# Kernel optimization log

Measured on AMD Instinct MI355X. Metric: run time of the kernel, lower is better.

Reference implementation:

```python
import jax, jax.numpy as jnp
import numpy as np

B, C, N = 2, 6, 2048      # batch, channels (xyz+3 extra), points per cloud
K, NS = 64, 32            # top-k keypoints, ball-query group size
D = 32                    # deep feature dim (num_feat)
RADIUS = 1.0              # ball query radius (sample_and_group)
VR, VS = 1.0, 0.4         # voxelize range / step -> 6^3 = 216 candidates


def setup_inputs() -> dict:
    key = jax.random.key(0)
    ks = jax.random.split(key, 16)
    rn = lambda k, s, sc=1.0: jax.random.normal(k, s, dtype=jnp.float32) * sc
    Q, _ = jnp.linalg.qr(jax.random.normal(ks[2], (3, 3), dtype=jnp.float32))
    return {
        "src_pts": rn(ks[0], (B, C, N)),
        "tgt_pts": rn(ks[1], (B, C, N)),
        "R_init": Q,
        "t_init": rn(ks[3], (1, 3), 0.1),
        "W1": rn(ks[4], (C, 64), 0.2), "b1": jnp.zeros((64,), jnp.float32),
        "W2": rn(ks[5], (64, D), 0.2), "b2": jnp.zeros((D,), jnp.float32),
        "Wwl": rn(ks[6], (D, 1), 0.2), "bwl": jnp.zeros((1,), jnp.float32),
        "W3": rn(ks[7], (3 + D, 64), 0.2), "b3": jnp.zeros((64,), jnp.float32),
        "W4": rn(ks[8], (64, D), 0.2), "b4": jnp.zeros((D,), jnp.float32),
    }


def _fe(pts, W1, b1, W2, b2):
    # feat_extraction_layer: shared point-wise MLP. pts [B,C,N] -> xyz [B,N,3], feat [B,N,D]
    x = jnp.transpose(pts, (0, 2, 1))
    xyz = x[..., :3]
    f = jax.nn.relu(x @ W1 + b1)
    f = jax.nn.relu(f @ W2 + b2)
    return xyz, f


def _index_points(pts, idx):
    # pts [B,N,D], idx [B,K,S] -> [B,K,S,D]
    b = pts.shape[0]
    return pts[jnp.arange(b)[:, None, None], idx]


def _sqdist(a, b):
    # a [B,M,3], b [B,N,3] -> [B,M,N]
    return (jnp.sum(a * a, -1)[:, :, None] + jnp.sum(b * b, -1)[:, None, :]
            - 2.0 * jnp.einsum('bmd,bnd->bmn', a, b))


def reference(src_pts, tgt_pts, R_init, t_init, W1, b1, W2, b2, Wwl, bwl, W3, b3, W4, b4):
    b = src_pts.shape[0]
    # FE1 on source
    src_xyz, src_feat = _fe(src_pts, W1, b1, W2, b2)
    # weighting_layer: per-point saliency -> top-K keypoint indices
    w = (src_feat @ Wwl + bwl)[..., 0]                    # [B,N]
    _, kidx = jax.lax.top_k(w, K)                          # [B,K]
    src_T = jnp.transpose(src_pts, (0, 2, 1))              # [B,N,C]
    src_keypts = jnp.take_along_axis(src_T, kidx[:, :, None], axis=1)  # [B,K,C]
    centers = src_keypts[..., :3]
    # sample_and_group: ball query NS nearest-within-radius around each keypoint
    d2 = _sqdist(centers, src_xyz)                         # [B,K,N]
    negd, nn = jax.lax.top_k(-d2, NS)
    group_idx = jnp.where(-negd <= RADIUS ** 2, nn, nn[:, :, :1])
    grouped_xyz = _index_points(src_xyz, group_idx)        # [B,K,NS,3]
    keyfeats = _index_points(src_feat, group_idx)          # [B,K,NS,D]
    src_cat = jnp.concatenate([grouped_xyz - centers[:, :, None, :], keyfeats], -1)
    # FE1 on target
    tgt_xyz, tgt_feat = _fe(tgt_pts, W1, b1, W2, b2)
    # transform keypoints with initial pose, voxelize into candidate grid
    xform = jnp.einsum('ij,bkj->bki', R_init, centers) + t_init
    g = jnp.arange(int(2 * VR / VS) + 1, dtype=jnp.float32) * VS - VR   # 6 steps
    gx, gy, gz = jnp.meshgrid(g, g, g, indexing='ij')
    offs = jnp.stack([gx.ravel(), gy.ravel(), gz.ravel()], -1)          # [216,3]
    cand = xform[:, :, None, :] + offs                      # [B,K,216,3]
    nc = offs.shape[0]
    cand_flat = cand.reshape(b, K * nc, 3)
    # nearest target point per candidate -> gathered deep feature + relative offset
    d2t = _sqdist(cand_flat, tgt_xyz)                       # [B,K*216,N] (dominant buffer)
    nnt = jnp.argmin(d2t, axis=-1)                          # [B,K*216]
    nn_xyz = jnp.take_along_axis(tgt_xyz, nnt[:, :, None], axis=1)
    nn_feat = jnp.take_along_axis(tgt_feat, nnt[:, :, None], axis=1)
    rel = (nn_xyz - cand_flat).reshape(b, K, nc, 3)
    tgt_cat = jnp.concatenate([rel, nn_feat.reshape(b, K, nc, D)], -1)
    # DFE: shared MLP; src branch max-pools over the NS group
    dfe = lambda x: jax.nn.relu(jax.nn.relu(x @ W3 + b3) @ W4 + b4)
    src_dfe = jnp.max(dfe(src_cat), axis=2)                 # [B,K,D]
    tgt_dfe = dfe(tgt_cat)                                  # [B,K,216,D]
    # cpg: similarity -> softmax over candidates -> weighted centroid
    sim = jnp.einsum('bkd,bkcd->bkc', src_dfe, tgt_dfe)
    attn = jax.nn.softmax(sim, axis=-1)
    vcp = jnp.einsum('bkc,bkcd->bkd', attn, cand)           # [B,K,3]
    return src_keypts, vcp
```

## Files before the change

### kernel.cpp

```cpp
#include <hip/hip_runtime.h>
#include <math.h>

#define BB_ 2
#define CC_ 6
#define NN_ 2048
#define KK_ 64
#define NS_ 32
#define DD_ 32
#define NC_ 216
#define HH_ 64

#define OFF_SRC_PACK 0
#define OFF_TGT_PACK 16384
#define OFF_SRC_FEAT 32768
#define OFF_TGT_FEAT 163840
#define OFF_W        294912
#define OFF_CENTERS  299008
#define OFF_XFORM    299392
#define OFF_SRCDFE   299776
#define OFF_NNT      303872

__device__ __forceinline__ unsigned sortable_f32(float f) {
    unsigned u = __float_as_uint(f);
    return (u & 0x80000000u) ? ~u : (u | 0x80000000u);
}
__device__ __forceinline__ float unsortable_f32(unsigned s) {
    unsigned u = (s & 0x80000000u) ? (s ^ 0x80000000u) : ~s;
    return __uint_as_float(u);
}

__device__ __forceinline__ unsigned long long wave_sort64_asc(unsigned long long key, int lane) {
#pragma unroll
    for (int k = 2; k <= 64; k <<= 1) {
#pragma unroll
        for (int j = k >> 1; j > 0; j >>= 1) {
            unsigned long long other = __shfl_xor(key, j);
            bool lower = (lane & j) == 0;
            bool asc = (lane & k) == 0;
            bool takemin = (lower == asc);
            unsigned long long mn = key < other ? key : other;
            unsigned long long mx = key < other ? other : key;
            key = takemin ? mn : mx;
        }
    }
    return key;
}

__device__ __forceinline__ unsigned long long merge_keep_min64(unsigned long long a, unsigned long long b, int lane) {
    unsigned long long br = __shfl(b, 63 - lane);
    unsigned long long m = a < br ? a : br;
#pragma unroll
    for (int j = 32; j > 0; j >>= 1) {
        unsigned long long other = __shfl_xor(m, j);
        bool lower = (lane & j) == 0;
        unsigned long long mn = m < other ? m : other;
        unsigned long long mx = m < other ? other : m;
        m = lower ? mn : mx;
    }
    return m;
}

__device__ __forceinline__ void block_select64_16w(unsigned long long kA, unsigned long long kB,
                                                   unsigned long long* runs, int tid) {
    int w = tid >> 6, lane = tid & 63;
    kA = wave_sort64_asc(kA, lane);
    kB = wave_sort64_asc(kB, lane);
    unsigned long long m = merge_keep_min64(kA, kB, lane);
    runs[w * 64 + lane] = m;
    __syncthreads();
#pragma unroll
    for (int lvl = 8; lvl >= 1; lvl >>= 1) {
        unsigned long long r = 0;
        if (w < lvl) {
            unsigned long long a = runs[w * 64 + lane];
            unsigned long long b = runs[(w + lvl) * 64 + lane];
            r = merge_keep_min64(a, b, lane);
        }
        __syncthreads();
        if (w < lvl) runs[w * 64 + lane] = r;
        __syncthreads();
    }
}

__global__ void fe_kernel(const float* __restrict__ src, const float* __restrict__ tgt,
                          const float* __restrict__ W1, const float* __restrict__ b1,
                          const float* __restrict__ W2, const float* __restrict__ b2,
                          const float* __restrict__ Wwl, const float* __restrict__ bwl,
                          float* __restrict__ ws) {
    int tid = blockIdx.x * blockDim.x + threadIdx.x;
    if (tid >= 2 * BB_ * NN_) return;
    int cloud = tid / (BB_ * NN_);
    int r = tid - cloud * BB_ * NN_;
    int b = r / NN_, n = r % NN_;
    const float* pts = cloud ? tgt : src;
    float x[CC_];
#pragma unroll
    for (int c = 0; c < CC_; ++c) x[c] = pts[(b * CC_ + c) * NN_ + n];
    float bb;
    {
#pragma clang fp contract(off)
        bb = (x[0] * x[0] + x[1] * x[1]) + x[2] * x[2];
    }
    float4* pack = (float4*)(ws + (cloud ? OFF_TGT_PACK : OFF_SRC_PACK));
    pack[b * NN_ + n] = make_float4(x[0], x[1], x[2], bb);

    float h[HH_];
#pragma unroll
    for (int t = 0; t < HH_; ++t) {
        float s = b1[t];
#pragma unroll
        for (int c = 0; c < CC_; ++c) s += x[c] * W1[c * HH_ + t];
        h[t] = fmaxf(s, 0.f);
    }
    float* feat = ws + (cloud ? OFF_TGT_FEAT : OFF_SRC_FEAT) + (size_t)(b * NN_ + n) * DD_;
    float wsum = 0.f;
#pragma unroll 4
    for (int d = 0; d < DD_; ++d) {
        float s = b2[d];
#pragma unroll
        for (int t = 0; t < HH_; ++t) s += h[t] * W2[t * DD_ + d];
        s = fmaxf(s, 0.f);
        feat[d] = s;
        wsum += s * Wwl[d];
    }
    if (cloud == 0) (ws + OFF_W)[b * NN_ + n] = wsum + bwl[0];
}

__global__ void topk_kernel(const float* __restrict__ src, const float* __restrict__ R,
                            const float* __restrict__ t, float* __restrict__ ws,
                            float* __restrict__ out) {
    __shared__ unsigned long long runs[16 * 64];
    int b = blockIdx.x;
    int tid = threadIdx.x, w = tid >> 6, lane = tid & 63;
    const float* wv = ws + OFF_W + b * NN_;
    int jA = w * 128 + lane, jB = jA + 64;
    unsigned long long kA = ((unsigned long long)(~sortable_f32(wv[jA])) << 32) | (unsigned)jA;
    unsigned long long kB = ((unsigned long long)(~sortable_f32(wv[jB])) << 32) | (unsigned)jB;
    block_select64_16w(kA, kB, runs, tid);
    if (tid < KK_) {
        int bi = (int)(runs[tid] & 0xFFFFFFFFu);
        float c3[3];
#pragma unroll
        for (int c = 0; c < CC_; ++c) {
            float v = src[(b * CC_ + c) * NN_ + bi];
            out[(b * KK_ + tid) * CC_ + c] = v;
            if (c < 3) c3[c] = v;
        }
        float* cen = ws + OFF_CENTERS + (b * KK_ + tid) * 3;
        cen[0] = c3[0]; cen[1] = c3[1]; cen[2] = c3[2];
        float* xf = ws + OFF_XFORM + (b * KK_ + tid) * 3;
#pragma unroll
        for (int i = 0; i < 3; ++i) {
#pragma clang fp contract(off)
            xf[i] = ((R[i * 3 + 0] * c3[0] + R[i * 3 + 1] * c3[1]) + R[i * 3 + 2] * c3[2]) + t[i];
        }
    }
}

__global__ __launch_bounds__(576) void mid_kernel(const float* __restrict__ W3, const float* __restrict__ b3,
                                                  const float* __restrict__ W4, const float* __restrict__ b4,
                                                  float* __restrict__ ws) {
    __shared__ union U {
        float4 pk[NN_];
        struct {
            unsigned long long runs[8 * 64];
            float hs[NS_][HH_];
            float outs[NS_][DD_];
        } s;
    } u;
    int blk = blockIdx.x;
    int tid = threadIdx.x;
    if (blk < 2 * BB_ * KK_) {
        int bk = blk >> 1;
        int half = blk & 1;
        int b = bk / KK_;
        const float4* pack = (const float4*)(ws + OFF_TGT_PACK) + b * NN_;
        for (int j = tid; j < NN_; j += 576) {
            u.pk[j ^ ((j >> 6) & 7)] = pack[j];
        }
        const float* xf = ws + OFF_XFORM + bk * 3;
        float x0 = xf[0], x1 = xf[1], x2 = xf[2];
        __syncthreads();

        int lg = tid >> 5;
        int chunk = tid & 31;
        int grp = half * 18 + lg;
        int ix = grp / 6, iy = grp % 6;
        float cx = x0 + (ix * 0.4f - 1.0f);
        float cy = x1 + (iy * 0.4f - 1.0f);
        float cxy2;
        {
#pragma clang fp contract(off)
            cxy2 = cx * cx + cy * cy;
        }
        float m2x = -2.0f * cx, m2y = -2.0f * cy;
        float aaz[6], m2z[6];
#pragma unroll
        for (int z = 0; z < 6; ++z) {
            float cz = x2 + (z * 0.4f - 1.0f);
            {
#pragma clang fp contract(off)
                aaz[z] = cxy2 + cz * cz;
            }
            m2z[z] = -2.0f * cz;
        }
        float bv[6];
        int bi[6];
#pragma unroll
        for (int z = 0; z < 6; ++z) { bv[z] = INFINITY; bi[z] = 0; }
        int base = chunk * 64;
        int sw = chunk & 7;
        for (int i = 0; i < 64; ++i) {
            int j = base + i;
            float4 p = u.pk[base + (i ^ sw)];
            float txy;
            {
#pragma clang fp contract(off)
                txy = m2x * p.x + m2y * p.y;
            }
#pragma unroll
            for (int z = 0; z < 6; ++z) {
                float d2;
                {
#pragma clang fp contract(off)
                    d2 = (aaz[z] + p.w) + (txy + m2z[z] * p.z);
                }
                if (d2 < bv[z]) { bv[z] = d2; bi[z] = j; }
            }
        }
        int* nnt = (int*)ws + OFF_NNT + bk * NC_ + grp * 6;
#pragma unroll
        for (int z = 0; z < 6; ++z) {
            unsigned long long key = ((unsigned long long)sortable_f32(bv[z]) << 32) | (unsigned)bi[z];
#pragma unroll
            for (int m = 1; m <= 16; m <<= 1) {
                unsigned long long other = __shfl_xor(key, m);
                key = other < key ? other : key;
            }
            if (chunk == 0) nnt[z] = (int)(key & 0xFFFFFFFFu);
        }
    } else {
        int bk = blk - 2 * BB_ * KK_;
        int b = bk / KK_;
        int w = tid >> 6, lane = tid & 63;
        const float* cen = ws + OFF_CENTERS + bk * 3;
        float c0 = cen[0], c1 = cen[1], c2 = cen[2];
        float aa;
        {
#pragma clang fp contract(off)
            aa = (c0 * c0 + c1 * c1) + c2 * c2;
        }
        float m2x = -2.0f * c0, m2y = -2.0f * c1, m2z = -2.0f * c2;
        const float4* pack = (const float4*)(ws + OFF_SRC_PACK) + b * NN_;
        if (w < 8) {
            unsigned long long k4[4];
#pragma unroll
            for (int q = 0; q < 4; ++q) {
                int j = w * 256 + q * 64 + lane;
                float4 p = pack[j];
                float d2;
                {
#pragma clang fp contract(off)
                    d2 = (aa + p.w) + ((m2x * p.x + m2y * p.y) + m2z * p.z);
                }
                k4[q] = ((unsigned long long)sortable_f32(d2) << 32) | (unsigned)j;
            }
            unsigned long long m1 = merge_keep_min64(wave_sort64_asc(k4[0], lane),
                                                     wave_sort64_asc(k4[1], lane), lane);
            unsigned long long m2 = merge_keep_min64(wave_sort64_asc(k4[2], lane),
                                                     wave_sort64_asc(k4[3], lane), lane);
            u.s.runs[w * 64 + lane] = merge_keep_min64(m1, m2, lane);
        }
        __syncthreads();
#pragma unroll
        for (int lvl = 4; lvl >= 1; lvl >>= 1) {
            unsigned long long r = 0;
            if (w < lvl) {
                r = merge_keep_min64(u.s.runs[w * 64 + lane], u.s.runs[(w + lvl) * 64 + lane], lane);
            }
            __syncthreads();
            if (w < lvl) u.s.runs[w * 64 + lane] = r;
            __syncthreads();
        }
        const float* feats = ws + OFF_SRC_FEAT + (size_t)b * NN_ * DD_;
        unsigned long long key0 = u.s.runs[0];
        if (w < 8) {
#pragma unroll
            for (int ss = 0; ss < 4; ++ss) {
                int s = w * 4 + ss;
                unsigned long long key = u.s.runs[s];
                float dd = unsortable_f32((unsigned)(key >> 32));
                int j = (dd <= 1.0f) ? (int)(key & 0xFFFFFFFFu) : (int)(key0 & 0xFFFFFFFFu);
                float4 p = pack[j];
                float r0 = p.x - c0, r1 = p.y - c1, r2 = p.z - c2;
                const float* f = feats + (size_t)j * DD_;
                float acc = b3[lane] + r0 * W3[0 * HH_ + lane] + r1 * W3[1 * HH_ + lane] + r2 * W3[2 * HH_ + lane];
#pragma unroll 8
                for (int d = 0; d < DD_; ++d) acc += f[d] * W3[(3 + d) * HH_ + lane];
                u.s.hs[s][lane] = fmaxf(acc, 0.f);
            }
        }
        __syncthreads();
        for (int idx = tid; idx < NS_ * DD_; idx += 576) {
            int s2 = idx >> 5, di = idx & 31;
            float o = b4[di];
#pragma unroll 8
            for (int t2 = 0; t2 < HH_; ++t2) o += u.s.hs[s2][t2] * W4[t2 * DD_ + di];
            u.s.outs[s2][di] = fmaxf(o, 0.f);
        }
        __syncthreads();
        if (tid < DD_) {
            float m = -INFINITY;
#pragma unroll 8
            for (int s = 0; s < NS_; ++s) m = fmaxf(m, u.s.outs[s][tid]);
            (ws + OFF_SRCDFE)[bk * DD_ + tid] = m;
        }
    }
}

__global__ void simvcp_kernel(const float* __restrict__ W3, const float* __restrict__ b3,
                              const float* __restrict__ W4, const float* __restrict__ b4,
                              float* __restrict__ ws, float* __restrict__ out) {
    __shared__ float sims[NC_];
    int bk = blockIdx.x;
    int b = bk / KK_;
    int tid = threadIdx.x;
    const float* xf = ws + OFF_XFORM + bk * 3;
    if (tid < NC_) {
        int c = tid;
        int ix = c / 36, iy = (c / 6) % 6, iz = c % 6;
        float cx = xf[0] + (ix * 0.4f - 1.0f);
        float cy = xf[1] + (iy * 0.4f - 1.0f);
        float cz = xf[2] + (iz * 0.4f - 1.0f);
        int bi = ((const int*)ws)[OFF_NNT + bk * NC_ + c];
        float4 p = ((const float4*)(ws + OFF_TGT_PACK))[b * NN_ + bi];
        float x[3 + DD_];
        x[0] = p.x - cx; x[1] = p.y - cy; x[2] = p.z - cz;
        const float* f = ws + OFF_TGT_FEAT + ((size_t)b * NN_ + bi) * DD_;
#pragma unroll
        for (int d = 0; d < DD_; ++d) x[3 + d] = f[d];
        float o[DD_];
#pragma unroll
        for (int d = 0; d < DD_; ++d) o[d] = b4[d];
        for (int t = 0; t < HH_; ++t) {
            float acc = b3[t];
#pragma unroll
            for (int cc = 0; cc < 3 + DD_; ++cc) acc += x[cc] * W3[cc * HH_ + t];
            float ht = fmaxf(acc, 0.f);
#pragma unroll
            for (int d = 0; d < DD_; ++d) o[d] += ht * W4[t * DD_ + d];
        }
        const float* sd = ws + OFF_SRCDFE + bk * DD_;
        float sim = 0.f;
#pragma unroll
        for (int d = 0; d < DD_; ++d) sim += fmaxf(o[d], 0.f) * sd[d];
        sims[c] = sim;
    }
    __syncthreads();
    if (tid < 64) {
        int lane = tid;
        float m = -INFINITY;
        for (int c = lane; c < NC_; c += 64) m = fmaxf(m, sims[c]);
#pragma unroll
        for (int sh = 32; sh; sh >>= 1) m = fmaxf(m, __shfl_xor(m, sh));
        float se = 0.f, v0 = 0.f, v1 = 0.f, v2 = 0.f;
        for (int c = lane; c < NC_; c += 64) {
            float e = expf(sims[c] - m);
            int ix = c / 36, iy = (c / 6) % 6, iz = c % 6;
            se += e;
            v0 += e * (xf[0] + (ix * 0.4f - 1.0f));
            v1 += e * (xf[1] + (iy * 0.4f - 1.0f));
            v2 += e * (xf[2] + (iz * 0.4f - 1.0f));
        }
#pragma unroll
        for (int sh = 32; sh; sh >>= 1) {
            se += __shfl_xor(se, sh);
            v0 += __shfl_xor(v0, sh);
            v1 += __shfl_xor(v1, sh);
            v2 += __shfl_xor(v2, sh);
        }
        if (lane == 0) {
            float inv = 1.0f / se;
            float* oo = out + BB_ * KK_ * CC_ + bk * 3;
            oo[0] = v0 * inv;
            oo[1] = v1 * inv;
            oo[2] = v2 * inv;
        }
    }
}

extern "C" void kernel_launch(void* const* d_in, const int* in_sizes, int n_in,
                              void* d_out, int out_size, void* d_ws, size_t ws_size,
                              hipStream_t stream) {
    const float* src = (const float*)d_in[0];
    const float* tgt = (const float*)d_in[1];
    const float* R   = (const float*)d_in[2];
    const float* t   = (const float*)d_in[3];
    const float* W1  = (const float*)d_in[4];
    const float* b1  = (const float*)d_in[5];
    const float* W2  = (const float*)d_in[6];
    const float* b2  = (const float*)d_in[7];
    const float* Wwl = (const float*)d_in[8];
    const float* bwl = (const float*)d_in[9];
    const float* W3  = (const float*)d_in[10];
    const float* b3  = (const float*)d_in[11];
    const float* W4  = (const float*)d_in[12];
    const float* b4  = (const float*)d_in[13];
    float* ws  = (float*)d_ws;
    float* out = (float*)d_out;

    fe_kernel<<<(2 * BB_ * NN_ + 127) / 128, 128, 0, stream>>>(src, tgt, W1, b1, W2, b2, Wwl, bwl, ws);
    topk_kernel<<<BB_, 1024, 0, stream>>>(src, R, t, ws, out);
    mid_kernel<<<2 * BB_ * KK_ + BB_ * KK_, 576, 0, stream>>>(W3, b3, W4, b4, ws);
    simvcp_kernel<<<BB_ * KK_, 256, 0, stream>>>(W3, b3, W4, b4, ws, out);
}
```

Baseline: 82.53 us.

## Fuse four stage kernels into one cooperative kernel with grid syncs

Merges feature extraction, top-k selection, target nearest-neighbour search, source grouping/DFE and the similarity/softmax stage into a single cooperatively launched kernel of 256 blocks of 576 threads, separated by grid.sync barriers. The aim is to remove the launch gaps between the four separate kernels. The source-grouping work, which previously ran in its own blocks concurrently with the NN search, now runs after the NN search in half of the same blocks, so that part is serialized. Top-k now uses 8 waves of 4 keys each instead of 16 waves. The old four-kernel path is kept as a fallback if the cooperative launch fails. The merged kernel also risks higher register pressure under the 576-thread launch bound, plus the cost of each grid-wide barrier.

```diff
diff --git a/kernel.cpp b/kernel.cpp
--- a/kernel.cpp
+++ b/kernel.cpp
@@ -1,5 +1,8 @@
 #include <hip/hip_runtime.h>
+#include <hip/hip_cooperative_groups.h>
 #include <math.h>
+
+namespace cg = cooperative_groups;
 
 #define BB_ 2
 #define CC_ 6
@@ -60,25 +63,335 @@
     return m;
 }
 
-__device__ __forceinline__ void block_select64_16w(unsigned long long kA, unsigned long long kB,
-                                                   unsigned long long* runs, int tid) {
-    int w = tid >> 6, lane = tid & 63;
-    kA = wave_sort64_asc(kA, lane);
-    kB = wave_sort64_asc(kB, lane);
-    unsigned long long m = merge_keep_min64(kA, kB, lane);
-    runs[w * 64 + lane] = m;
+
+struct MegaLds {
+    union {
+        float4 pk[NN_];
+        struct {
+            unsigned long long runs[8 * 64];
+            float hs[NS_][HH_];
+            float outs[NS_][DD_];
+        } s;
+        float sims[NC_];
+    };
+};
+
+__global__ __launch_bounds__(576) void mega_kernel(
+        const float* __restrict__ src, const float* __restrict__ tgt,
+        const float* __restrict__ R, const float* __restrict__ t,
+        const float* __restrict__ W1, const float* __restrict__ b1,
+        const float* __restrict__ W2, const float* __restrict__ b2,
+        const float* __restrict__ Wwl, const float* __restrict__ bwl,
+        const float* __restrict__ W3, const float* __restrict__ b3,
+        const float* __restrict__ W4, const float* __restrict__ b4,
+        float* __restrict__ ws, float* __restrict__ out) {
+    cg::grid_group grid = cg::this_grid();
+    __shared__ MegaLds u;
+    int blk = blockIdx.x;
+    int tid = threadIdx.x;
+
+    {
+        int g = blk * 576 + tid;
+        if (g < 2 * BB_ * NN_) {
+            int cloud = g / (BB_ * NN_);
+            int r = g - cloud * BB_ * NN_;
+            int b = r / NN_, n = r % NN_;
+            const float* pts = cloud ? tgt : src;
+            float x[CC_];
+#pragma unroll
+            for (int c = 0; c < CC_; ++c) x[c] = pts[(b * CC_ + c) * NN_ + n];
+            float bb;
+            {
+#pragma clang fp contract(off)
+                bb = (x[0] * x[0] + x[1] * x[1]) + x[2] * x[2];
+            }
+            float4* pack = (float4*)(ws + (cloud ? OFF_TGT_PACK : OFF_SRC_PACK));
+            pack[b * NN_ + n] = make_float4(x[0], x[1], x[2], bb);
+            float h[HH_];
+#pragma unroll
+            for (int tt = 0; tt < HH_; ++tt) {
+                float s = b1[tt];
+#pragma unroll
+                for (int c = 0; c < CC_; ++c) s += x[c] * W1[c * HH_ + tt];
+                h[tt] = fmaxf(s, 0.f);
+            }
+            float* feat = ws + (cloud ? OFF_TGT_FEAT : OFF_SRC_FEAT) + (size_t)(b * NN_ + n) * DD_;
+            float wsum = 0.f;
+#pragma unroll 4
+            for (int d = 0; d < DD_; ++d) {
+                float s = b2[d];
+#pragma unroll
+                for (int tt = 0; tt < HH_; ++tt) s += h[tt] * W2[tt * DD_ + d];
+                s = fmaxf(s, 0.f);
+                feat[d] = s;
+                wsum += s * Wwl[d];
+            }
+            if (cloud == 0) (ws + OFF_W)[b * NN_ + n] = wsum + bwl[0];
+        }
+    }
+    grid.sync();
+
+    if (blk < BB_) {
+        int b = blk;
+        int w = tid >> 6, lane = tid & 63;
+        const float* wv = ws + OFF_W + b * NN_;
+        if (w < 8) {
+            unsigned long long k4[4];
+#pragma unroll
+            for (int q = 0; q < 4; ++q) {
+                int j = w * 256 + q * 64 + lane;
+                k4[q] = ((unsigned long long)(~sortable_f32(wv[j])) << 32) | (unsigned)j;
+            }
+            unsigned long long m1 = merge_keep_min64(wave_sort64_asc(k4[0], lane),
+                                                     wave_sort64_asc(k4[1], lane), lane);
+            unsigned long long m2 = merge_keep_min64(wave_sort64_asc(k4[2], lane),
+                                                     wave_sort64_asc(k4[3], lane), lane);
+            u.s.runs[w * 64 + lane] = merge_keep_min64(m1, m2, lane);
+        }
+        __syncthreads();
+#pragma unroll
+        for (int lvl = 4; lvl >= 1; lvl >>= 1) {
+            unsigned long long r = 0;
+            if (w < lvl) r = merge_keep_min64(u.s.runs[w * 64 + lane], u.s.runs[(w + lvl) * 64 + lane], lane);
+            __syncthreads();
+            if (w < lvl) u.s.runs[w * 64 + lane] = r;
+            __syncthreads();
+        }
+        if (tid < KK_) {
+            int bi = (int)(u.s.runs[tid] & 0xFFFFFFFFu);
+            float c3[3];
+#pragma unroll
+            for (int c = 0; c < CC_; ++c) {
+                float v = src[(b * CC_ + c) * NN_ + bi];
+                out[(b * KK_ + tid) * CC_ + c] = v;
+                if (c < 3) c3[c] = v;
+            }
+            float* cen = ws + OFF_CENTERS + (b * KK_ + tid) * 3;
+            cen[0] = c3[0]; cen[1] = c3[1]; cen[2] = c3[2];
+            float* xf = ws + OFF_XFORM + (b * KK_ + tid) * 3;
+#pragma unroll
+            for (int i = 0; i < 3; ++i) {
+#pragma clang fp contract(off)
+                xf[i] = ((R[i * 3 + 0] * c3[0] + R[i * 3 + 1] * c3[1]) + R[i * 3 + 2] * c3[2]) + t[i];
+            }
+        }
+    }
+    grid.sync();
+
+    {
+        int bk = blk >> 1;
+        int half = blk & 1;
+        int b = bk / KK_;
+        const float4* pack = (const float4*)(ws + OFF_TGT_PACK) + b * NN_;
+        for (int j = tid; j < NN_; j += 576) {
+            u.pk[j ^ ((j >> 6) & 7)] = pack[j];
+        }
+        const float* xf = ws + OFF_XFORM + bk * 3;
+        float x0 = xf[0], x1 = xf[1], x2 = xf[2];
+        __syncthreads();
+
+        int lg = tid >> 5;
+        int chunk = tid & 31;
+        int grp = half * 18 + lg;
+        int ix = grp / 6, iy = grp % 6;
+        float cx = x0 + (ix * 0.4f - 1.0f);
+        float cy = x1 + (iy * 0.4f - 1.0f);
+        float cxy2;
+        {
+#pragma clang fp contract(off)
+            cxy2 = cx * cx + cy * cy;
+        }
+        float m2x = -2.0f * cx, m2y = -2.0f * cy;
+        float aaz[6], m2z[6];
+#pragma unroll
+        for (int z = 0; z < 6; ++z) {
+            float cz = x2 + (z * 0.4f - 1.0f);
+            {
+#pragma clang fp contract(off)
+                aaz[z] = cxy2 + cz * cz;
+            }
+            m2z[z] = -2.0f * cz;
+        }
+        float bv[6];
+        int bi[6];
+#pragma unroll
+        for (int z = 0; z < 6; ++z) { bv[z] = INFINITY; bi[z] = 0; }
+        int base = chunk * 64;
+        int sw = chunk & 7;
+        for (int i = 0; i < 64; ++i) {
+            int j = base + i;
+            float4 p = u.pk[base + (i ^ sw)];
+            float txy;
+            {
+#pragma clang fp contract(off)
+                txy = m2x * p.x + m2y * p.y;
+            }
+#pragma unroll
+            for (int z = 0; z < 6; ++z) {
+                float d2;
+                {
+#pragma clang fp contract(off)
+                    d2 = (aaz[z] + p.w) + (txy + m2z[z] * p.z);
+                }
+                if (d2 < bv[z]) { bv[z] = d2; bi[z] = j; }
+            }
+        }
+        int* nnt = (int*)ws + OFF_NNT + bk * NC_ + grp * 6;
+#pragma unroll
+        for (int z = 0; z < 6; ++z) {
+            unsigned long long key = ((unsigned long long)sortable_f32(bv[z]) << 32) | (unsigned)bi[z];
+#pragma unroll
+            for (int m = 1; m <= 16; m <<= 1) {
+                unsigned long long other = __shfl_xor(key, m);
+                key = other < key ? other : key;
+            }
+            if (chunk == 0) nnt[z] = (int)(key & 0xFFFFFFFFu);
+        }
+    }
     __syncthreads();
-#pragma unroll
-    for (int lvl = 8; lvl >= 1; lvl >>= 1) {
-        unsigned long long r = 0;
-        if (w < lvl) {
-            unsigned long long a = runs[w * 64 + lane];
-            unsigned long long b = runs[(w + lvl) * 64 + lane];
-            r = merge_keep_min64(a, b, lane);
-        }
-        __syncthreads();
-        if (w < lvl) runs[w * 64 + lane] = r;
-        __syncthreads();
+
+    if (blk >= BB_ * KK_) {
+        int bk = blk - BB_ * KK_;
+        int b = bk / KK_;
+        int w = tid >> 6, lane = tid & 63;
+        const float* cen = ws + OFF_CENTERS + bk * 3;
+        float c0 = cen[0], c1 = cen[1], c2 = cen[2];
+        float aa;
+        {
+#pragma clang fp contract(off)
+            aa = (c0 * c0 + c1 * c1) + c2 * c2;
+        }
+        float m2x = -2.0f * c0, m2y = -2.0f * c1, m2z = -2.0f * c2;
+        const float4* pack = (const float4*)(ws + OFF_SRC_PACK) + b * NN_;
+        if (w < 8) {
+            unsigned long long k4[4];
+#pragma unroll
+            for (int q = 0; q < 4; ++q) {
+                int j = w * 256 + q * 64 + lane;
+                float4 p = pack[j];
+                float d2;
+                {
+#pragma clang fp contract(off)
+                    d2 = (aa + p.w) + ((m2x * p.x + m2y * p.y) + m2z * p.z);
+                }
+                k4[q] = ((unsigned long long)sortable_f32(d2) << 32) | (unsigned)j;
+            }
+            unsigned long long m1 = merge_keep_min64(wave_sort64_asc(k4[0], lane),
+                                                     wave_sort64_asc(k4[1], lane), lane);
+            unsigned long long m2 = merge_keep_min64(wave_sort64_asc(k4[2], lane),
+                                                     wave_sort64_asc(k4[3], lane), lane);
+            u.s.runs[w * 64 + lane] = merge_keep_min64(m1, m2, lane);
+        }
+        __syncthreads();
+#pragma unroll
+        for (int lvl = 4; lvl >= 1; lvl >>= 1) {
+            unsigned long long r = 0;
+            if (w < lvl) r = merge_keep_min64(u.s.runs[w * 64 + lane], u.s.runs[(w + lvl) * 64 + lane], lane);
+            __syncthreads();
+            if (w < lvl) u.s.runs[w * 64 + lane] = r;
+            __syncthreads();
+        }
+        const float* feats = ws + OFF_SRC_FEAT + (size_t)b * NN_ * DD_;
+        unsigned long long key0 = u.s.runs[0];
+        if (w < 8) {
+#pragma unroll
+            for (int ss = 0; ss < 4; ++ss) {
+                int s = w * 4 + ss;
+                unsigned long long key = u.s.runs[s];
+                float dd = unsortable_f32((unsigned)(key >> 32));
+                int j = (dd <= 1.0f) ? (int)(key & 0xFFFFFFFFu) : (int)(key0 & 0xFFFFFFFFu);
+                float4 p = pack[j];
+                float r0 = p.x - c0, r1 = p.y - c1, r2 = p.z - c2;
+                const float* f = feats + (size_t)j * DD_;
+                float acc = b3[lane] + r0 * W3[0 * HH_ + lane] + r1 * W3[1 * HH_ + lane] + r2 * W3[2 * HH_ + lane];
+#pragma unroll 8
+                for (int d = 0; d < DD_; ++d) acc += f[d] * W3[(3 + d) * HH_ + lane];
+                u.s.hs[s][lane] = fmaxf(acc, 0.f);
+            }
+        }
+        __syncthreads();
+        for (int idx = tid; idx < NS_ * DD_; idx += 576) {
+            int s2 = idx >> 5, di = idx & 31;
+            float o = b4[di];
+#pragma unroll 8
+            for (int t2 = 0; t2 < HH_; ++t2) o += u.s.hs[s2][t2] * W4[t2 * DD_ + di];
+            u.s.outs[s2][di] = fmaxf(o, 0.f);
+        }
+        __syncthreads();
+        if (tid < DD_) {
+            float m = -INFINITY;
+#pragma unroll 8
+            for (int s = 0; s < NS_; ++s) m = fmaxf(m, u.s.outs[s][tid]);
+            (ws + OFF_SRCDFE)[bk * DD_ + tid] = m;
+        }
+    }
+    grid.sync();
+
+    if (blk < BB_ * KK_) {
+        int bk = blk;
+        int b = bk / KK_;
+        const float* xf = ws + OFF_XFORM + bk * 3;
+        if (tid < NC_) {
+            int c = tid;
+            int ix = c / 36, iy = (c / 6) % 6, iz = c % 6;
+            float cx = xf[0] + (ix * 0.4f - 1.0f);
+            float cy = xf[1] + (iy * 0.4f - 1.0f);
+            float cz = xf[2] + (iz * 0.4f - 1.0f);
+            int bi = ((const int*)ws)[OFF_NNT + bk * NC_ + c];
+            float4 p = ((const float4*)(ws + OFF_TGT_PACK))[b * NN_ + bi];
+            float x[3 + DD_];
+            x[0] = p.x - cx; x[1] = p.y - cy; x[2] = p.z - cz;
+            const float* f = ws + OFF_TGT_FEAT + ((size_t)b * NN_ + bi) * DD_;
+#pragma unroll
+            for (int d = 0; d < DD_; ++d) x[3 + d] = f[d];
+            float o[DD_];
+#pragma unroll
+            for (int d = 0; d < DD_; ++d) o[d] = b4[d];
+            for (int tt = 0; tt < HH_; ++tt) {
+                float acc = b3[tt];
+#pragma unroll
+                for (int cc = 0; cc < 3 + DD_; ++cc) acc += x[cc] * W3[cc * HH_ + tt];
+                float ht = fmaxf(acc, 0.f);
+#pragma unroll
+                for (int d = 0; d < DD_; ++d) o[d] += ht * W4[tt * DD_ + d];
+            }
+            const float* sd = ws + OFF_SRCDFE + bk * DD_;
+            float sim = 0.f;
+#pragma unroll
+            for (int d = 0; d < DD_; ++d) sim += fmaxf(o[d], 0.f) * sd[d];
+            u.sims[c] = sim;
+        }
+        __syncthreads();
+        if (tid < 64) {
+            int lane = tid;
+            float m = -INFINITY;
+            for (int c = lane; c < NC_; c += 64) m = fmaxf(m, u.sims[c]);
+#pragma unroll
+            for (int sh = 32; sh; sh >>= 1) m = fmaxf(m, __shfl_xor(m, sh));
+            float se = 0.f, v0 = 0.f, v1 = 0.f, v2 = 0.f;
+            for (int c = lane; c < NC_; c += 64) {
+                float e = expf(u.sims[c] - m);
+                int ix = c / 36, iy = (c / 6) % 6, iz = c % 6;
+                se += e;
+                v0 += e * (xf[0] + (ix * 0.4f - 1.0f));
+                v1 += e * (xf[1] + (iy * 0.4f - 1.0f));
+                v2 += e * (xf[2] + (iz * 0.4f - 1.0f));
+            }
+#pragma unroll
+            for (int sh = 32; sh; sh >>= 1) {
+                se += __shfl_xor(se, sh);
+                v0 += __shfl_xor(v0, sh);
+                v1 += __shfl_xor(v1, sh);
+                v2 += __shfl_xor(v2, sh);
+            }
+            if (lane == 0) {
+                float inv = 1.0f / se;
+                float* oo = out + BB_ * KK_ * CC_ + bk * 3;
+                oo[0] = v0 * inv;
+                oo[1] = v1 * inv;
+                oo[2] = v2 * inv;
+            }
+        }
     }
 }
 
@@ -103,7 +416,6 @@
     }
     float4* pack = (float4*)(ws + (cloud ? OFF_TGT_PACK : OFF_SRC_PACK));
     pack[b * NN_ + n] = make_float4(x[0], x[1], x[2], bb);
-
     float h[HH_];
 #pragma unroll
     for (int t = 0; t < HH_; ++t) {
@@ -129,14 +441,30 @@
 __global__ void topk_kernel(const float* __restrict__ src, const float* __restrict__ R,
                             const float* __restrict__ t, float* __restrict__ ws,
                             float* __restrict__ out) {
-    __shared__ unsigned long long runs[16 * 64];
+    __shared__ unsigned long long runs[8 * 64];
     int b = blockIdx.x;
     int tid = threadIdx.x, w = tid >> 6, lane = tid & 63;
     const float* wv = ws + OFF_W + b * NN_;
-    int jA = w * 128 + lane, jB = jA + 64;
-    unsigned long long kA = ((unsigned long long)(~sortable_f32(wv[jA])) << 32) | (unsigned)jA;
-    unsigned long long kB = ((unsigned long long)(~sortable_f32(wv[jB])) << 32) | (unsigned)jB;
-    block_select64_16w(kA, kB, runs, tid);
+    if (w < 8) {
+        unsigned long long k4[4];
+#pragma unroll
+        for (int q = 0; q < 4; ++q) {
+            int j = w * 256 + q * 64 + lane;
+            k4[q] = ((unsigned long long)(~sortable_f32(wv[j])) << 32) | (unsigned)j;
+        }
+        unsigned long long m1 = merge_keep_min64(wave_sort64_asc(k4[0], lane), wave_sort64_asc(k4[1], lane), lane);
+        unsigned long long m2 = merge_keep_min64(wave_sort64_asc(k4[2], lane), wave_sort64_asc(k4[3], lane), lane);
+        runs[w * 64 + lane] = merge_keep_min64(m1, m2, lane);
+    }
+    __syncthreads();
+#pragma unroll
+    for (int lvl = 4; lvl >= 1; lvl >>= 1) {
+        unsigned long long r = 0;
+        if (w < lvl) r = merge_keep_min64(runs[w * 64 + lane], runs[(w + lvl) * 64 + lane], lane);
+        __syncthreads();
+        if (w < lvl) runs[w * 64 + lane] = r;
+        __syncthreads();
+    }
     if (tid < KK_) {
         int bi = (int)(runs[tid] & 0xFFFFFFFFu);
         float c3[3];
@@ -160,14 +488,7 @@
 __global__ __launch_bounds__(576) void mid_kernel(const float* __restrict__ W3, const float* __restrict__ b3,
                                                   const float* __restrict__ W4, const float* __restrict__ b4,
                                                   float* __restrict__ ws) {
-    __shared__ union U {
-        float4 pk[NN_];
-        struct {
-            unsigned long long runs[8 * 64];
-            float hs[NS_][HH_];
-            float outs[NS_][DD_];
-        } s;
-    } u;
+    __shared__ MegaLds u;
     int blk = blockIdx.x;
     int tid = threadIdx.x;
     if (blk < 2 * BB_ * KK_) {
@@ -175,13 +496,10 @@
         int half = blk & 1;
         int b = bk / KK_;
         const float4* pack = (const float4*)(ws + OFF_TGT_PACK) + b * NN_;
-        for (int j = tid; j < NN_; j += 576) {
-            u.pk[j ^ ((j >> 6) & 7)] = pack[j];
-        }
+        for (int j = tid; j < NN_; j += 576) u.pk[j ^ ((j >> 6) & 7)] = pack[j];
         const float* xf = ws + OFF_XFORM + bk * 3;
         float x0 = xf[0], x1 = xf[1], x2 = xf[2];
         __syncthreads();
-
         int lg = tid >> 5;
         int chunk = tid & 31;
         int grp = half * 18 + lg;
@@ -265,19 +583,15 @@
                 }
                 k4[q] = ((unsigned long long)sortable_f32(d2) << 32) | (unsigned)j;
             }
-            unsigned long long m1 = merge_keep_min64(wave_sort64_asc(k4[0], lane),
-                                                     wave_sort64_asc(k4[1], lane), lane);
-            unsigned long long m2 = merge_keep_min64(wave_sort64_asc(k4[2], lane),
-                                                     wave_sort64_asc(k4[3], lane), lane);
+            unsigned long long m1 = merge_keep_min64(wave_sort64_asc(k4[0], lane), wave_sort64_asc(k4[1], lane), lane);
+            unsigned long long m2 = merge_keep_min64(wave_sort64_asc(k4[2], lane), wave_sort64_asc(k4[3], lane), lane);
             u.s.runs[w * 64 + lane] = merge_keep_min64(m1, m2, lane);
         }
         __syncthreads();
 #pragma unroll
         for (int lvl = 4; lvl >= 1; lvl >>= 1) {
             unsigned long long r = 0;
-            if (w < lvl) {
-                r = merge_keep_min64(u.s.runs[w * 64 + lane], u.s.runs[(w + lvl) * 64 + lane], lane);
-            }
+            if (w < lvl) r = merge_keep_min64(u.s.runs[w * 64 + lane], u.s.runs[(w + lvl) * 64 + lane], lane);
             __syncthreads();
             if (w < lvl) u.s.runs[w * 64 + lane] = r;
             __syncthreads();
@@ -409,8 +723,17 @@
     float* ws  = (float*)d_ws;
     float* out = (float*)d_out;
 
-    fe_kernel<<<(2 * BB_ * NN_ + 127) / 128, 128, 0, stream>>>(src, tgt, W1, b1, W2, b2, Wwl, bwl, ws);
-    topk_kernel<<<BB_, 1024, 0, stream>>>(src, R, t, ws, out);
-    mid_kernel<<<2 * BB_ * KK_ + BB_ * KK_, 576, 0, stream>>>(W3, b3, W4, b4, ws);
-    simvcp_kernel<<<BB_ * KK_, 256, 0, stream>>>(W3, b3, W4, b4, ws, out);
-}
+    void* args[] = {(void*)&src, (void*)&tgt, (void*)&R, (void*)&t,
+                    (void*)&W1, (void*)&b1, (void*)&W2, (void*)&b2,
+                    (void*)&Wwl, (void*)&bwl, (void*)&W3, (void*)&b3,
+                    (void*)&W4, (void*)&b4, (void*)&ws, (void*)&out};
+    hipError_t e = hipLaunchCooperativeKernel((const void*)mega_kernel,
+                                              dim3(2 * BB_ * KK_), dim3(576),
+                                              args, 0, stream);
+    if (e != hipSuccess) {
+        fe_kernel<<<(2 * BB_ * NN_ + 127) / 128, 128, 0, stream>>>(src, tgt, W1, b1, W2, b2, Wwl, bwl, ws);
+        topk_kernel<<<BB_, 576, 0, stream>>>(src, R, t, ws, out);
+        mid_kernel<<<2 * BB_ * KK_ + BB_ * KK_, 576, 0, stream>>>(W3, b3, W4, b4, ws);
+        simvcp_kernel<<<BB_ * KK_, 256, 0, stream>>>(W3, b3, W4, b4, ws, out);
+    }
+}
```

After: 164.7 us. +99.6%, slower.
